# Kernel tuning notes

Hardware: AMD Instinct MI355X
Metric: run time of the kernel (lower is better)

The kernel has to match this reference:

```python
import jax, jax.numpy as jnp
import numpy as np

SCALE = 64.0
MARGIN = 0.5
COS_M = float(np.cos(MARGIN))
SIN_M = float(np.sin(MARGIN))
TH = float(np.cos(np.pi - MARGIN))
MM = float(np.sin(np.pi - MARGIN) * MARGIN)
B, D, C = 1024, 512, 50000


def setup_inputs() -> dict:
    key = jax.random.key(0)
    k1, k2, k3 = jax.random.split(key, 3)
    embeddings = jax.random.normal(k1, (B, D), dtype=jnp.float32)
    labels = jax.random.randint(k2, (B,), 0, C, dtype=jnp.int32)
    # xavier_uniform over (num_classes, embedding_dim)
    limit = float(np.sqrt(6.0 / (C + D)))
    weight = jax.random.uniform(k3, (C, D), dtype=jnp.float32, minval=-limit, maxval=limit)
    return {"embeddings": embeddings, "labels": labels, "weight": weight}


def _l2norm(x, axis=-1, eps=1e-12):
    # matches F.normalize(p=2): x / max(||x||, eps)
    n = jnp.sqrt(jnp.sum(x * x, axis=axis, keepdims=True))
    return x / jnp.maximum(n, eps)


def reference(embeddings, labels, weight):
    e = _l2norm(embeddings, axis=1)          # [B, D]
    w = _l2norm(weight, axis=1)              # [C, D]
    cosine = jnp.einsum('bd,cd->bc', e, w)   # [B, C]
    sine = jnp.sqrt(1.0 - jnp.clip(cosine * cosine, 0.0, 1.0))
    phi = cosine * COS_M - sine * SIN_M
    phi = jnp.where(cosine > TH, phi, cosine - MM)
    one_hot = jax.nn.one_hot(labels, cosine.shape[1], dtype=cosine.dtype)
    logits = SCALE * (one_hot * phi + (1.0 - one_hot) * cosine)
    # cross_entropy with integer labels, mean reduction
    logp = jax.nn.log_softmax(logits, axis=1)
    nll = -jnp.take_along_axis(logp, labels[:, None].astype(jnp.int32), axis=1)[:, 0]
    return jnp.mean(nll)
```

## Files before the change

kernel.cpp:

```cpp
#include <hip/hip_runtime.h>
#include <hip/hip_bf16.h>
#include <cstdint>

#define BB 1024
#define DD 512
#define CC 50000
#define NTN 782
#define GROUPS 98
#define NTPB 8
#define NBLK 784
#define PSTRIDE 196
#define SCALE_F 64.0f
#define COS_M_F 0.87758256189037276f
#define SIN_M_F 0.47942553860420301f
#define TH_F   (-0.87758256189037276f)
#define MM_F   0.23971276930210156f

typedef __attribute__((ext_vector_type(4))) int i32x4;
typedef __attribute__((ext_vector_type(8))) char char8;

#define OFF_PS   ((size_t)0)
#define OFF_LABV (OFF_PS + (size_t)BB*PSTRIDE*4)
#define OFF_NLL  (OFF_LABV + 8192)
#define OFF_ES   (OFF_NLL + 4096)
#define OFF_WS   (OFF_ES + 4096)
#define OFF_EI8  (OFF_WS + 204800)
#define OFF_WI8  (OFF_EI8 + (size_t)BB*DD)

__global__ void norm_e_i8_kernel(const float* __restrict__ e,
                                 char* __restrict__ ei8, float* __restrict__ es) {
    const int b = blockIdx.x;
    const int l = threadIdx.x;
    const float4* row = reinterpret_cast<const float4*>(e + (size_t)b * DD);
    float4 v0 = row[l * 2 + 0];
    float4 v1 = row[l * 2 + 1];
    float ss = v0.x*v0.x + v0.y*v0.y + v0.z*v0.z + v0.w*v0.w
             + v1.x*v1.x + v1.y*v1.y + v1.z*v1.z + v1.w*v1.w;
    float mx = fmaxf(fmaxf(fmaxf(fabsf(v0.x), fabsf(v0.y)), fmaxf(fabsf(v0.z), fabsf(v0.w))),
                     fmaxf(fmaxf(fabsf(v1.x), fabsf(v1.y)), fmaxf(fabsf(v1.z), fabsf(v1.w))));
    #pragma unroll
    for (int m = 1; m < 64; m <<= 1) {
        ss += __shfl_xor(ss, m);
        mx = fmaxf(mx, __shfl_xor(mx, m));
    }
    float nrm = fmaxf(sqrtf(ss), 1e-12f);
    float ma  = fmaxf(mx, 1e-20f);
    float qs  = 127.0f / ma;
    if (l == 0) es[b] = ma / (127.0f * nrm);
    char8 q;
    q[0]=(char)__float2int_rn(v0.x*qs); q[1]=(char)__float2int_rn(v0.y*qs);
    q[2]=(char)__float2int_rn(v0.z*qs); q[3]=(char)__float2int_rn(v0.w*qs);
    q[4]=(char)__float2int_rn(v1.x*qs); q[5]=(char)__float2int_rn(v1.y*qs);
    q[6]=(char)__float2int_rn(v1.z*qs); q[7]=(char)__float2int_rn(v1.w*qs);
    *reinterpret_cast<char8*>(ei8 + (size_t)b * DD + l * 8) = q;
}

__global__ void wnorm_i8_kernel(const float* __restrict__ w,
                                char* __restrict__ wi8, float* __restrict__ wsc) {
    const int row = blockIdx.x * 4 + (threadIdx.x >> 6);
    const int l = threadIdx.x & 63;
    const float4* r = reinterpret_cast<const float4*>(w + (size_t)row * DD);
    float4 v0 = r[l * 2 + 0];
    float4 v1 = r[l * 2 + 1];
    float ss = v0.x*v0.x + v0.y*v0.y + v0.z*v0.z + v0.w*v0.w
             + v1.x*v1.x + v1.y*v1.y + v1.z*v1.z + v1.w*v1.w;
    float mx = fmaxf(fmaxf(fmaxf(fabsf(v0.x), fabsf(v0.y)), fmaxf(fabsf(v0.z), fabsf(v0.w))),
                     fmaxf(fmaxf(fabsf(v1.x), fabsf(v1.y)), fmaxf(fabsf(v1.z), fabsf(v1.w))));
    #pragma unroll
    for (int m = 1; m < 64; m <<= 1) {
        ss += __shfl_xor(ss, m);
        mx = fmaxf(mx, __shfl_xor(mx, m));
    }
    float nrm = fmaxf(sqrtf(ss), 1e-12f);
    float ma  = fmaxf(mx, 1e-20f);
    float qs  = 127.0f / ma;
    if (l == 0) wsc[row] = ma / (127.0f * nrm);
    char8 q;
    q[0]=(char)__float2int_rn(v0.x*qs); q[1]=(char)__float2int_rn(v0.y*qs);
    q[2]=(char)__float2int_rn(v0.z*qs); q[3]=(char)__float2int_rn(v0.w*qs);
    q[4]=(char)__float2int_rn(v1.x*qs); q[5]=(char)__float2int_rn(v1.y*qs);
    q[6]=(char)__float2int_rn(v1.z*qs); q[7]=(char)__float2int_rn(v1.w*qs);
    *reinterpret_cast<char8*>(wi8 + (size_t)row * DD + l * 8) = q;
}

__global__ __launch_bounds__(512, 4) void arc_gemm_i8_kernel(
        const char* __restrict__ ei8,
        const char* __restrict__ wi8,
        const float* __restrict__ es,
        const float* __restrict__ wsc,
        float* __restrict__ part_s)
{
    __shared__ __align__(16) char lds[2][32768];

    const int t   = threadIdx.x;
    const int wid = t >> 6;
    const int wm  = wid >> 1;
    const int wn  = wid & 1;
    const int l   = t & 63;
    const int r16 = l & 15;
    const int kg  = l >> 4;

    const int bid  = blockIdx.x;
    const int bidp = (bid & 7) * GROUPS + (bid >> 3);
    const int mt = bidp & 7;
    const int g  = bidp >> 3;
    const int m0 = mt * 128;
    const int nt0 = g * NTPB;
    const int cnt = min(NTPB, NTN - nt0);

    i32x4 af[2][8];
    #pragma unroll
    for (int fm = 0; fm < 2; ++fm)
        #pragma unroll
        for (int kk = 0; kk < 8; ++kk)
            af[fm][kk] = *reinterpret_cast<const i32x4*>(
                ei8 + (size_t)(m0 + wm * 32 + fm * 16 + r16) * DD + kk * 64 + kg * 16);

    float se_r[2][4];
    #pragma unroll
    for (int fm = 0; fm < 2; ++fm)
        #pragma unroll
        for (int j = 0; j < 4; ++j)
            se_r[fm][j] = es[m0 + wm * 32 + fm * 16 + kg * 4 + j];

    float rs[2][4];
    #pragma unroll
    for (int fm = 0; fm < 2; ++fm)
        #pragma unroll
        for (int j = 0; j < 4; ++j) rs[fm][j] = 0.f;

    auto stageB = [&](int buf, int nt) {
        #pragma unroll
        for (int i = 0; i < 4; ++i) {
            int flat = (i * 512 + t) * 16;
            int kk2  = flat >> 13;
            int row  = (flat >> 7) & 63;
            int col  = flat & 127;
            int scol = col ^ ((row & 7) << 4);
            int cls  = nt * 64 + row;
            if (cls > CC - 1) cls = CC - 1;
            const char* src = wi8 + (size_t)cls * DD + kk2 * 128 + scol;
            __builtin_amdgcn_global_load_lds(
                (const __attribute__((address_space(1))) void*)src,
                (__attribute__((address_space(3))) void*)(&lds[buf][flat]),
                16, 0, 0);
        }
    };

    stageB(0, nt0);
    asm volatile("s_waitcnt vmcnt(0)" ::: "memory");
    __builtin_amdgcn_s_barrier();

    for (int i = 0; i < cnt; ++i) {
        const int buf = i & 1;
        if (i + 1 < cnt) stageB(buf ^ 1, nt0 + i + 1);

        i32x4 acc[2][2];
        #pragma unroll
        for (int fm = 0; fm < 2; ++fm)
            #pragma unroll
            for (int fn = 0; fn < 2; ++fn) acc[fm][fn] = (i32x4){0, 0, 0, 0};
        #pragma unroll
        for (int kk = 0; kk < 8; ++kk) {
            i32x4 b[2];
            #pragma unroll
            for (int fn = 0; fn < 2; ++fn) {
                int row = wn * 32 + fn * 16 + r16;
                int off = (kk >> 1) * 8192 + row * 128
                        + (((kk & 1) * 64 + kg * 16) ^ ((row & 7) << 4));
                b[fn] = *reinterpret_cast<const i32x4*>(&lds[buf][off]);
            }
            #pragma unroll
            for (int fm = 0; fm < 2; ++fm)
                #pragma unroll
                for (int fn = 0; fn < 2; ++fn)
                    acc[fm][fn] = __builtin_amdgcn_mfma_i32_16x16x64_i8(af[fm][kk], b[fn], acc[fm][fn], 0, 0, 0);
        }

        const int nt = nt0 + i;
        #pragma unroll
        for (int fn = 0; fn < 2; ++fn) {
            int col = nt * 64 + wn * 32 + fn * 16 + r16;
            float sw = wsc[col > CC - 1 ? CC - 1 : col];
            bool ok = (col < CC);
            #pragma unroll
            for (int fm = 0; fm < 2; ++fm)
                #pragma unroll
                for (int j = 0; j < 4; ++j) {
                    float cosv = (float)acc[fm][fn][j] * se_r[fm][j] * sw;
                    float e = __expf(SCALE_F * cosv - SCALE_F);
                    rs[fm][j] += ok ? e : 0.f;
                }
        }

        asm volatile("s_waitcnt vmcnt(0)" ::: "memory");
        __builtin_amdgcn_s_barrier();
    }

    #pragma unroll
    for (int fm = 0; fm < 2; ++fm) {
        #pragma unroll
        for (int j = 0; j < 4; ++j) {
            float v = rs[fm][j];
            #pragma unroll
            for (int mk = 1; mk < 16; mk <<= 1) v += __shfl_xor(v, mk);
            if (r16 == 0) {
                int grow = m0 + wm * 32 + fm * 16 + kg * 4 + j;
                part_s[(size_t)grow * PSTRIDE + g * 2 + wn] = v;
            }
        }
    }
}

__global__ void labfix_kernel(const char* __restrict__ ei8, const char* __restrict__ wi8,
                              const float* __restrict__ es, const float* __restrict__ wsc,
                              const int* __restrict__ labels, float* __restrict__ labv) {
    const int b = blockIdx.x;
    const int l = threadIdx.x;
    const int lab = labels[b];
    char8 a = *reinterpret_cast<const char8*>(ei8 + (size_t)b * DD + l * 8);
    char8 w = *reinterpret_cast<const char8*>(wi8 + (size_t)lab * DD + l * 8);
    int d = 0;
    #pragma unroll
    for (int k = 0; k < 8; ++k) d += (int)a[k] * (int)w[k];
    #pragma unroll
    for (int m = 1; m < 64; m <<= 1) d += __shfl_xor(d, m);
    if (l == 0) {
        float cosv = (float)d * es[b] * wsc[lab];
        float logit = SCALE_F * cosv;
        float sub = __expf(logit - SCALE_F);
        float c2 = fminf(fmaxf(cosv * cosv, 0.f), 1.f);
        float phi = cosv * COS_M_F - sqrtf(1.f - c2) * SIN_M_F;
        phi = (cosv > TH_F) ? phi : (cosv - MM_F);
        float ml = SCALE_F * phi;
        labv[2 * b]     = ml;
        labv[2 * b + 1] = __expf(ml - SCALE_F) - sub;
    }
}

__global__ void row_lse_kernel(const float* __restrict__ part_s,
                               const float* __restrict__ labv,
                               float* __restrict__ nll) {
    const int row = blockIdx.x;
    const int t = threadIdx.x;
    const float* ps = part_s + (size_t)row * PSTRIDE;
    float S = 0.f;
    for (int i = t; i < PSTRIDE; i += 256) S += ps[i];
    #pragma unroll
    for (int m = 1; m < 64; m <<= 1) S += __shfl_xor(S, m);
    __shared__ float reds[4];
    if ((t & 63) == 0) reds[t >> 6] = S;
    __syncthreads();
    if (t == 0) {
        float Sf = reds[0] + reds[1] + reds[2] + reds[3] + labv[2 * row + 1];
        nll[row] = -(labv[2 * row] - SCALE_F - logf(Sf));
    }
}

__global__ void mean_kernel(const float* __restrict__ nll, float* __restrict__ out) {
    const int t = threadIdx.x;
    float v = nll[t];
    #pragma unroll
    for (int m = 1; m < 64; m <<= 1) v += __shfl_xor(v, m);
    __shared__ float red[16];
    if ((t & 63) == 0) red[t >> 6] = v;
    __syncthreads();
    if (t == 0) {
        float s = 0.f;
        #pragma unroll
        for (int i = 0; i < 16; ++i) s += red[i];
        out[0] = s * (1.0f / BB);
    }
}

extern "C" void kernel_launch(void* const* d_in, const int* in_sizes, int n_in,
                              void* d_out, int out_size, void* d_ws, size_t ws_size,
                              hipStream_t stream) {
    const float* emb    = (const float*)d_in[0];
    const int*   labels = (const int*)d_in[1];
    const float* wgt    = (const float*)d_in[2];
    float* out = (float*)d_out;
    char* ws = (char*)d_ws;

    float* ps     = (float*)(ws + OFF_PS);
    float* labv   = (float*)(ws + OFF_LABV);
    float* nll    = (float*)(ws + OFF_NLL);
    float* es     = (float*)(ws + OFF_ES);
    float* wsc    = (float*)(ws + OFF_WS);
    char*  ei8    = (char*)(ws + OFF_EI8);
    char*  wi8    = (char*)(ws + OFF_WI8);

    norm_e_i8_kernel<<<BB, 64, 0, stream>>>(emb, ei8, es);
    wnorm_i8_kernel<<<CC / 4, 256, 0, stream>>>(wgt, wi8, wsc);
    arc_gemm_i8_kernel<<<NBLK, 512, 0, stream>>>(ei8, wi8, es, wsc, ps);
    labfix_kernel<<<BB, 64, 0, stream>>>(ei8, wi8, es, wsc, labels, labv);
    row_lse_kernel<<<BB, 256, 0, stream>>>(ps, labv, nll);
    mean_kernel<<<1, 1024, 0, stream>>>(nll, out);
}
```

Before: 84.03 us.

## Fuse quantization kernels, rebalance GEMM grid, and reduce via atomics

Merges the embedding and weight quantization kernels into one launch, which also zeroes the row-sum and output buffers. The GEMM grid goes from 784 blocks of 8 n-tiles to 512 blocks of 12-13 n-tiles. Each GEMM block now adds its per-row partial sums into a global row-sum array with atomics, replacing the partial-sum buffer. The row log-sum-exp and mean kernels are folded into the label-fix kernel, which accumulates the mean with an atomic. This cuts six launches to three and drops two small tail kernels, at the cost of atomic contention and a summation order that is no longer deterministic.

```diff
diff --git a/kernel.cpp b/kernel.cpp
--- a/kernel.cpp
+++ b/kernel.cpp
@@ -6,10 +6,7 @@
 #define DD 512
 #define CC 50000
 #define NTN 782
-#define GROUPS 98
-#define NTPB 8
-#define NBLK 784
-#define PSTRIDE 196
+#define NBLK 512
 #define SCALE_F 64.0f
 #define COS_M_F 0.87758256189037276f
 #define SIN_M_F 0.47942553860420301f
@@ -19,47 +16,30 @@
 typedef __attribute__((ext_vector_type(4))) int i32x4;
 typedef __attribute__((ext_vector_type(8))) char char8;
 
-#define OFF_PS   ((size_t)0)
-#define OFF_LABV (OFF_PS + (size_t)BB*PSTRIDE*4)
-#define OFF_NLL  (OFF_LABV + 8192)
-#define OFF_ES   (OFF_NLL + 4096)
+#define OFF_RS   ((size_t)0)
+#define OFF_ES   (OFF_RS + 4096)
 #define OFF_WS   (OFF_ES + 4096)
 #define OFF_EI8  (OFF_WS + 204800)
 #define OFF_WI8  (OFF_EI8 + (size_t)BB*DD)
 
-__global__ void norm_e_i8_kernel(const float* __restrict__ e,
-                                 char* __restrict__ ei8, float* __restrict__ es) {
-    const int b = blockIdx.x;
-    const int l = threadIdx.x;
-    const float4* row = reinterpret_cast<const float4*>(e + (size_t)b * DD);
-    float4 v0 = row[l * 2 + 0];
-    float4 v1 = row[l * 2 + 1];
-    float ss = v0.x*v0.x + v0.y*v0.y + v0.z*v0.z + v0.w*v0.w
-             + v1.x*v1.x + v1.y*v1.y + v1.z*v1.z + v1.w*v1.w;
-    float mx = fmaxf(fmaxf(fmaxf(fabsf(v0.x), fabsf(v0.y)), fmaxf(fabsf(v0.z), fabsf(v0.w))),
-                     fmaxf(fmaxf(fabsf(v1.x), fabsf(v1.y)), fmaxf(fabsf(v1.z), fabsf(v1.w))));
-    #pragma unroll
-    for (int m = 1; m < 64; m <<= 1) {
-        ss += __shfl_xor(ss, m);
-        mx = fmaxf(mx, __shfl_xor(mx, m));
-    }
-    float nrm = fmaxf(sqrtf(ss), 1e-12f);
-    float ma  = fmaxf(mx, 1e-20f);
-    float qs  = 127.0f / ma;
-    if (l == 0) es[b] = ma / (127.0f * nrm);
-    char8 q;
-    q[0]=(char)__float2int_rn(v0.x*qs); q[1]=(char)__float2int_rn(v0.y*qs);
-    q[2]=(char)__float2int_rn(v0.z*qs); q[3]=(char)__float2int_rn(v0.w*qs);
-    q[4]=(char)__float2int_rn(v1.x*qs); q[5]=(char)__float2int_rn(v1.y*qs);
-    q[6]=(char)__float2int_rn(v1.z*qs); q[7]=(char)__float2int_rn(v1.w*qs);
-    *reinterpret_cast<char8*>(ei8 + (size_t)b * DD + l * 8) = q;
-}
-
-__global__ void wnorm_i8_kernel(const float* __restrict__ w,
-                                char* __restrict__ wi8, float* __restrict__ wsc) {
-    const int row = blockIdx.x * 4 + (threadIdx.x >> 6);
-    const int l = threadIdx.x & 63;
-    const float4* r = reinterpret_cast<const float4*>(w + (size_t)row * DD);
+__global__ void quant_kernel(const float* __restrict__ emb, const float* __restrict__ wgt,
+                             char* __restrict__ ei8, float* __restrict__ es,
+                             char* __restrict__ wi8, float* __restrict__ wsc,
+                             float* __restrict__ rowsum, float* __restrict__ out) {
+    const int blk = blockIdx.x;
+    if (blk == 12756) {
+        const int t = threadIdx.x;
+        #pragma unroll
+        for (int i = 0; i < 4; ++i) rowsum[i * 256 + t] = 0.f;
+        if (t == 0) out[0] = 0.f;
+        return;
+    }
+    const int r4 = threadIdx.x >> 6;
+    const int l  = threadIdx.x & 63;
+    const bool isw = blk < 12500;
+    const int row = isw ? (blk * 4 + r4) : ((blk - 12500) * 4 + r4);
+    const float* src = (isw ? wgt : emb) + (size_t)row * DD;
+    const float4* r = reinterpret_cast<const float4*>(src);
     float4 v0 = r[l * 2 + 0];
     float4 v1 = r[l * 2 + 1];
     float ss = v0.x*v0.x + v0.y*v0.y + v0.z*v0.z + v0.w*v0.w
@@ -74,13 +54,13 @@
     float nrm = fmaxf(sqrtf(ss), 1e-12f);
     float ma  = fmaxf(mx, 1e-20f);
     float qs  = 127.0f / ma;
-    if (l == 0) wsc[row] = ma / (127.0f * nrm);
+    if (l == 0) (isw ? wsc : es)[row] = ma / (127.0f * nrm);
     char8 q;
     q[0]=(char)__float2int_rn(v0.x*qs); q[1]=(char)__float2int_rn(v0.y*qs);
     q[2]=(char)__float2int_rn(v0.z*qs); q[3]=(char)__float2int_rn(v0.w*qs);
     q[4]=(char)__float2int_rn(v1.x*qs); q[5]=(char)__float2int_rn(v1.y*qs);
     q[6]=(char)__float2int_rn(v1.z*qs); q[7]=(char)__float2int_rn(v1.w*qs);
-    *reinterpret_cast<char8*>(wi8 + (size_t)row * DD + l * 8) = q;
+    *reinterpret_cast<char8*>((isw ? wi8 : ei8) + (size_t)row * DD + l * 8) = q;
 }
 
 __global__ __launch_bounds__(512, 4) void arc_gemm_i8_kernel(
@@ -88,7 +68,7 @@
         const char* __restrict__ wi8,
         const float* __restrict__ es,
         const float* __restrict__ wsc,
-        float* __restrict__ part_s)
+        float* __restrict__ rowsum)
 {
     __shared__ __align__(16) char lds[2][32768];
 
@@ -101,12 +81,12 @@
     const int kg  = l >> 4;
 
     const int bid  = blockIdx.x;
-    const int bidp = (bid & 7) * GROUPS + (bid >> 3);
+    const int bidp = (bid & 7) * 64 + (bid >> 3);
     const int mt = bidp & 7;
-    const int g  = bidp >> 3;
+    const int s  = bidp >> 3;
     const int m0 = mt * 128;
-    const int nt0 = g * NTPB;
-    const int cnt = min(NTPB, NTN - nt0);
+    const int nt0 = (s < 14) ? s * 13 : 12 * s + 14;
+    const int cnt = (s < 14) ? 13 : 12;
 
     i32x4 af[2][8];
     #pragma unroll
@@ -206,15 +186,16 @@
             for (int mk = 1; mk < 16; mk <<= 1) v += __shfl_xor(v, mk);
             if (r16 == 0) {
                 int grow = m0 + wm * 32 + fm * 16 + kg * 4 + j;
-                part_s[(size_t)grow * PSTRIDE + g * 2 + wn] = v;
+                atomicAdd(&rowsum[grow], v);
             }
         }
     }
 }
 
-__global__ void labfix_kernel(const char* __restrict__ ei8, const char* __restrict__ wi8,
+__global__ void finish_kernel(const char* __restrict__ ei8, const char* __restrict__ wi8,
                               const float* __restrict__ es, const float* __restrict__ wsc,
-                              const int* __restrict__ labels, float* __restrict__ labv) {
+                              const int* __restrict__ labels,
+                              const float* __restrict__ rowsum, float* __restrict__ out) {
     const int b = blockIdx.x;
     const int l = threadIdx.x;
     const int lab = labels[b];
@@ -233,43 +214,9 @@
         float phi = cosv * COS_M_F - sqrtf(1.f - c2) * SIN_M_F;
         phi = (cosv > TH_F) ? phi : (cosv - MM_F);
         float ml = SCALE_F * phi;
-        labv[2 * b]     = ml;
-        labv[2 * b + 1] = __expf(ml - SCALE_F) - sub;
-    }
-}
-
-__global__ void row_lse_kernel(const float* __restrict__ part_s,
-                               const float* __restrict__ labv,
-                               float* __restrict__ nll) {
-    const int row = blockIdx.x;
-    const int t = threadIdx.x;
-    const float* ps = part_s + (size_t)row * PSTRIDE;
-    float S = 0.f;
-    for (int i = t; i < PSTRIDE; i += 256) S += ps[i];
-    #pragma unroll
-    for (int m = 1; m < 64; m <<= 1) S += __shfl_xor(S, m);
-    __shared__ float reds[4];
-    if ((t & 63) == 0) reds[t >> 6] = S;
-    __syncthreads();
-    if (t == 0) {
-        float Sf = reds[0] + reds[1] + reds[2] + reds[3] + labv[2 * row + 1];
-        nll[row] = -(labv[2 * row] - SCALE_F - logf(Sf));
-    }
-}
-
-__global__ void mean_kernel(const float* __restrict__ nll, float* __restrict__ out) {
-    const int t = threadIdx.x;
-    float v = nll[t];
-    #pragma unroll
-    for (int m = 1; m < 64; m <<= 1) v += __shfl_xor(v, m);
-    __shared__ float red[16];
-    if ((t & 63) == 0) red[t >> 6] = v;
-    __syncthreads();
-    if (t == 0) {
-        float s = 0.f;
-        #pragma unroll
-        for (int i = 0; i < 16; ++i) s += red[i];
-        out[0] = s * (1.0f / BB);
+        float Sf = rowsum[b] + __expf(ml - SCALE_F) - sub;
+        float nll = -(ml - SCALE_F - logf(Sf));
+        atomicAdd(out, nll * (1.0f / BB));
     }
 }
 
@@ -282,18 +229,13 @@
     float* out = (float*)d_out;
     char* ws = (char*)d_ws;
 
-    float* ps     = (float*)(ws + OFF_PS);
-    float* labv   = (float*)(ws + OFF_LABV);
-    float* nll    = (float*)(ws + OFF_NLL);
+    float* rowsum = (float*)(ws + OFF_RS);
     float* es     = (float*)(ws + OFF_ES);
     float* wsc    = (float*)(ws + OFF_WS);
     char*  ei8    = (char*)(ws + OFF_EI8);
     char*  wi8    = (char*)(ws + OFF_WI8);
 
-    norm_e_i8_kernel<<<BB, 64, 0, stream>>>(emb, ei8, es);
-    wnorm_i8_kernel<<<CC / 4, 256, 0, stream>>>(wgt, wi8, wsc);
-    arc_gemm_i8_kernel<<<NBLK, 512, 0, stream>>>(ei8, wi8, es, wsc, ps);
-    labfix_kernel<<<BB, 64, 0, stream>>>(ei8, wi8, es, wsc, labels, labv);
-    row_lse_kernel<<<BB, 256, 0, stream>>>(ps, labv, nll);
-    mean_kernel<<<1, 1024, 0, stream>>>(nll, out);
-}
+    quant_kernel<<<12757, 256, 0, stream>>>(emb, wgt, ei8, es, wi8, wsc, rowsum, out);
+    arc_gemm_i8_kernel<<<NBLK, 512, 0, stream>>>(ei8, wi8, es, wsc, rowsum);
+    finish_kernel<<<BB, 64, 0, stream>>>(ei8, wi8, es, wsc, labels, rowsum, out);
+}
```

New measurement: 80.72 us. 3.9% less time.
